# Kernel tuning notes

Measured on AMD Instinct MI355X. Metric: run time of the kernel, lower is better.

## Reference

```python
import jax, jax.numpy as jnp
import numpy as np

T = 16           # number of stochastic-computing cycles (sequential forward calls)
N = 2097152      # parallel stochastic lanes (flattened element count)
BUF_DEP = 4      # shift-register depth (default buf_dep)


def setup_inputs() -> dict:
    key = jax.random.key(0)
    k1, k2 = jax.random.split(key)
    # bitstreams: values in {0,1}, stored as float32 per bstype=torch.float
    dividend = jax.random.randint(k1, (T, N), 0, 2).astype(jnp.float32)
    divisor = jax.random.randint(k2, (T, N), 0, 2).astype(jnp.float32)
    # ShiftReg_init: sr[i] = i % 2, broadcast to input shape -> [BUF_DEP, N]
    sr_init = jnp.tile((jnp.arange(BUF_DEP) % 2).astype(jnp.float32)[:, None], (1, N))
    # 2-bit (log2(buf_dep)) 1-D Sobol sequence scaled to integers 0..3
    rng_table = jnp.array([0, 2, 3, 1], dtype=jnp.int32)
    return {"dividend": dividend, "divisor": divisor, "sr_init": sr_init, "rng_table": rng_table}


def reference(dividend, divisor, sr_init, rng_table):
    T_ = dividend.shape[0]
    buf_dep = sr_init.shape[0]
    # idx starts at 0 and increments each cycle; gather index = rng[idx % buf_dep]
    rng_idx = rng_table[jnp.arange(T_) % buf_dep]  # [T]

    def step(sr, xs):
        dvd, dvs, r = xs
        sel = (dvs == 1).astype(dvd.dtype)                     # divisor_eq_1
        hq = jax.lax.dynamic_index_in_dim(sr, r, axis=0, keepdims=False)  # historic_q [N]
        q = sel * dvd + (1 - sel) * hq                          # quotient [N]
        # ShiftReg push: new value at slot 0, others shift down, oldest dropped
        sr = jnp.concatenate([q[None], sr[:-1]], axis=0)
        return sr, q

    _, quotients = jax.lax.scan(step, sr_init, (dividend, divisor, rng_idx))
    return quotients  # [T, N]
```

## Files before the change

kernel.cpp:

```cpp
#include <hip/hip_runtime.h>
#include <stdint.h>


#define SC_T   16
#define SC_BUF 4
#define CHUNK  4
#define BLOCK  256

typedef float v4f __attribute__((ext_vector_type(4)));
typedef const __attribute__((address_space(1))) void glb_void;
typedef __attribute__((address_space(3))) void lds_void;

__global__ __launch_bounds__(BLOCK) void cordiv_kernel(
    const v4f* __restrict__ dividend,
    const v4f* __restrict__ divisor,
    const v4f* __restrict__ sr_init,
    const int* __restrict__ rng_table,
    v4f*       __restrict__ out,
    int n4)
{
    __shared__ v4f lds_dvd[CHUNK][BLOCK];
    __shared__ v4f lds_dvs[CHUNK][BLOCK];

    const int tid   = threadIdx.x;
    const int gid   = blockIdx.x * BLOCK + tid;
    const int wbase = tid & ~63;

    const int r0 = rng_table[0];
    const int r1 = rng_table[1];
    const int r2 = rng_table[2];
    const int r3 = rng_table[3];
    const int rtab[SC_BUF] = {r0, r1, r2, r3};

    v4f sr0 = sr_init[0 * n4 + gid];
    v4f sr1 = sr_init[1 * n4 + gid];
    v4f sr2 = sr_init[2 * n4 + gid];
    v4f sr3 = sr_init[3 * n4 + gid];

#pragma unroll
    for (int c = 0; c < SC_T / CHUNK; ++c) {
#pragma unroll
        for (int i = 0; i < CHUNK; ++i) {
            const int t = c * CHUNK + i;
            __builtin_amdgcn_global_load_lds(
                (glb_void*)(dividend + (size_t)t * n4 + gid),
                (lds_void*)&lds_dvd[i][wbase], 16, 0, 0);
            __builtin_amdgcn_global_load_lds(
                (glb_void*)(divisor + (size_t)t * n4 + gid),
                (lds_void*)&lds_dvs[i][wbase], 16, 0, 0);
        }

        asm volatile("s_waitcnt vmcnt(0)" ::: "memory");

#pragma unroll
        for (int i = 0; i < CHUNK; ++i) {
            const int t = c * CHUNK + i;
            const int r = rtab[t & (SC_BUF - 1)];

            const v4f dvd = lds_dvd[i][tid];
            const v4f dvs = lds_dvs[i][tid];

            const v4f hq = (r == 0) ? sr0 : (r == 1) ? sr1
                         : (r == 2) ? sr2 : sr3;

            v4f q;
            q.x = (dvs.x == 1.0f) ? dvd.x : hq.x;
            q.y = (dvs.y == 1.0f) ? dvd.y : hq.y;
            q.z = (dvs.z == 1.0f) ? dvd.z : hq.z;
            q.w = (dvs.w == 1.0f) ? dvd.w : hq.w;

            out[(size_t)t * n4 + gid] = q;

            sr3 = sr2; sr2 = sr1; sr1 = sr0; sr0 = q;
        }
    }
}

extern "C" void kernel_launch(void* const* d_in, const int* in_sizes, int n_in,
                              void* d_out, int out_size, void* d_ws, size_t ws_size,
                              hipStream_t stream) {
    const float* dividend = (const float*)d_in[0];
    const float* divisor  = (const float*)d_in[1];
    const float* sr_init  = (const float*)d_in[2];
    const int*   rng      = (const int*)d_in[3];
    float*       out      = (float*)d_out;

    const int n  = in_sizes[0] / SC_T;
    const int n4 = n / 4;

    const int grid = (n4 + BLOCK - 1) / BLOCK;

    cordiv_kernel<<<grid, BLOCK, 0, stream>>>(
        (const v4f*)dividend, (const v4f*)divisor,
        (const v4f*)sr_init, rng, (v4f*)out, n4);
}
```

Baseline: 338.9 us.

## Double-buffer LDS chunk loads with partial vmcnt waits

Splits the timestep loads into chunks of two and double-buffers them in LDS, issuing loads two chunks ahead and waiting only with a partial vmcnt count, so compute and stores overlap with outstanding global loads. The per-block LDS footprint stays the same. The wait count must also account for stores in flight, and a mistake there risks reading stale LDS data. The grid size now truncates instead of rounding up, which assumes n4 is a multiple of the block size.

```diff
diff --git a/kernel.cpp b/kernel.cpp
--- a/kernel.cpp
+++ b/kernel.cpp
@@ -3,13 +3,15 @@
 
 
 #define SC_T   16
-#define SC_BUF 4
-#define CHUNK  4
+#define CHUNK  2
+#define NCHNK  (SC_T / CHUNK)
 #define BLOCK  256
 
 typedef float v4f __attribute__((ext_vector_type(4)));
 typedef const __attribute__((address_space(1))) void glb_void;
 typedef __attribute__((address_space(3))) void lds_void;
+
+#define WAITN(c) (CHUNK * ((c) >= 1) + 2 * CHUNK * ((c) + 1 < NCHNK))
 
 __global__ __launch_bounds__(BLOCK) void cordiv_kernel(
     const v4f* __restrict__ dividend,
@@ -19,8 +21,8 @@
     v4f*       __restrict__ out,
     int n4)
 {
-    __shared__ v4f lds_dvd[CHUNK][BLOCK];
-    __shared__ v4f lds_dvs[CHUNK][BLOCK];
+    __shared__ v4f ldsD[2][CHUNK][BLOCK];
+    __shared__ v4f ldsS[2][CHUNK][BLOCK];
 
     const int tid   = threadIdx.x;
     const int gid   = blockIdx.x * BLOCK + tid;
@@ -30,35 +32,41 @@
     const int r1 = rng_table[1];
     const int r2 = rng_table[2];
     const int r3 = rng_table[3];
-    const int rtab[SC_BUF] = {r0, r1, r2, r3};
+    const int rtab[4] = {r0, r1, r2, r3};
 
     v4f sr0 = sr_init[0 * n4 + gid];
     v4f sr1 = sr_init[1 * n4 + gid];
     v4f sr2 = sr_init[2 * n4 + gid];
     v4f sr3 = sr_init[3 * n4 + gid];
+    asm volatile("" : "+v"(sr0), "+v"(sr1), "+v"(sr2), "+v"(sr3));
+
+#define ISSUE(c) do {                                                     \
+        _Pragma("unroll")                                                 \
+        for (int i = 0; i < CHUNK; ++i) {                                 \
+            const int t = (c) * CHUNK + i;                                \
+            __builtin_amdgcn_global_load_lds(                             \
+                (glb_void*)(dividend + (size_t)t * n4 + gid),             \
+                (lds_void*)&ldsD[(c) & 1][i][wbase], 16, 0, 0);           \
+            __builtin_amdgcn_global_load_lds(                             \
+                (glb_void*)(divisor + (size_t)t * n4 + gid),              \
+                (lds_void*)&ldsS[(c) & 1][i][wbase], 16, 0, 0);           \
+        }                                                                 \
+    } while (0)
+
+    ISSUE(0);
+    ISSUE(1);
 
 #pragma unroll
-    for (int c = 0; c < SC_T / CHUNK; ++c) {
-#pragma unroll
-        for (int i = 0; i < CHUNK; ++i) {
-            const int t = c * CHUNK + i;
-            __builtin_amdgcn_global_load_lds(
-                (glb_void*)(dividend + (size_t)t * n4 + gid),
-                (lds_void*)&lds_dvd[i][wbase], 16, 0, 0);
-            __builtin_amdgcn_global_load_lds(
-                (glb_void*)(divisor + (size_t)t * n4 + gid),
-                (lds_void*)&lds_dvs[i][wbase], 16, 0, 0);
-        }
-
-        asm volatile("s_waitcnt vmcnt(0)" ::: "memory");
+    for (int c = 0; c < NCHNK; ++c) {
+        asm volatile("s_waitcnt vmcnt(%c0)" :: "i"(WAITN(c)) : "memory");
 
 #pragma unroll
         for (int i = 0; i < CHUNK; ++i) {
             const int t = c * CHUNK + i;
-            const int r = rtab[t & (SC_BUF - 1)];
+            const int r = rtab[t & 3];
 
-            const v4f dvd = lds_dvd[i][tid];
-            const v4f dvs = lds_dvs[i][tid];
+            const v4f dvd = ldsD[c & 1][i][tid];
+            const v4f dvs = ldsS[c & 1][i][tid];
 
             const v4f hq = (r == 0) ? sr0 : (r == 1) ? sr1
                          : (r == 2) ? sr2 : sr3;
@@ -73,7 +81,10 @@
 
             sr3 = sr2; sr2 = sr1; sr1 = sr0; sr0 = q;
         }
+
+        if (c + 2 < NCHNK) ISSUE(c + 2);
     }
+#undef ISSUE
 }
 
 extern "C" void kernel_launch(void* const* d_in, const int* in_sizes, int n_in,
@@ -88,7 +99,7 @@
     const int n  = in_sizes[0] / SC_T;
     const int n4 = n / 4;
 
-    const int grid = (n4 + BLOCK - 1) / BLOCK;
+    const int grid = n4 / BLOCK;
 
     cordiv_kernel<<<grid, BLOCK, 0, stream>>>(
         (const v4f*)dividend, (const v4f*)divisor,
```

New measurement: 334.2 us. No clear change (-1.4%).
